# Kernel tuning notes

Measured on AMD Instinct MI355X. Metric: run time of the kernel, lower is better.

The kernel has to match this reference:

```python
import jax, jax.numpy as jnp
import numpy as np

B, T, V, E, Hd, NTAG = 16, 512, 32000, 100, 500, 32
PAD, SOS, EOS = 0, 1, 2
NEG = -10000.0


def _lstm_dir(xs, mask, Wih, Whh, b, h0, c0, reverse):
    # xs: [T,B,D]; mask: [T,B] bool. Packed-sequence semantics: at padded
    # steps the state is frozen and the output is zero (pad_packed fills 0).
    def step(carry, inp):
        h, c = carry
        x_t, m = inp
        g = x_t @ Wih.T + h @ Whh.T + b
        i, f, gg, o = jnp.split(g, 4, axis=-1)  # torch gate order i,f,g,o
        c_new = jax.nn.sigmoid(f) * c + jax.nn.sigmoid(i) * jnp.tanh(gg)
        h_new = jax.nn.sigmoid(o) * jnp.tanh(c_new)
        m_ = m[:, None]
        return (jnp.where(m_, h_new, h), jnp.where(m_, c_new, c)), jnp.where(m_, h_new, 0.0)
    _, ys = jax.lax.scan(step, (h0, c0), (xs, mask), reverse=reverse)
    return ys


def _forward(x, y0, embed_W, Wih0, Whh0, bih0, bhh0, Wih1, Whh1, bih1, bhh1, W_out, b_out, trans, h0, c0):
    maskb = x > 0                       # [B,T]
    maskf = maskb.astype(embed_W.dtype)
    mT = maskb.T                        # [T,B]
    xs = embed_W[x].transpose(1, 0, 2)  # [T,B,E]
    # layer 0 (bidirectional)
    f0 = _lstm_dir(xs, mT, Wih0[0], Whh0[0], bih0[0] + bhh0[0], h0[0], c0[0], False)
    b0 = _lstm_dir(xs, mT, Wih0[1], Whh0[1], bih0[1] + bhh0[1], h0[1], c0[1], True)
    l1 = jnp.concatenate([f0, b0], axis=-1)  # [T,B,1000]
    # layer 1 (dropout omitted: deterministic reference)
    f1 = _lstm_dir(l1, mT, Wih1[0], Whh1[0], bih1[0] + bhh1[0], h0[2], c0[2], False)
    b1 = _lstm_dir(l1, mT, Wih1[1], Whh1[1], bih1[1] + bhh1[1], h0[3], c0[3], True)
    hseq = jnp.concatenate([f1, b1], axis=-1).transpose(1, 0, 2)  # [B,T,1000]
    # emissions, masked exactly as in loss(): y = y * mask
    y = (hseq @ W_out.T + b_out) * maskf[:, :, None]  # [B,T,NTAG]
    # gold path score (crf_score_batch)
    y0e = jnp.concatenate([jnp.full((B, 1), SOS, y0.dtype), y0], axis=1)
    emit = jnp.take_along_axis(y, y0e[:, 1:, None], axis=2)[..., 0]
    tr = trans[y0e[:, 1:], y0e[:, :-1]] * maskf
    gold = jnp.sum(emit + tr, axis=1)  # [B]
    # log-partition (crf_forward_batch). Faithful to the original, including
    # the quirk that finished rows are overwritten with max_g score[b,g].
    init = jnp.full((B, NTAG), NEG, y.dtype).at[:, SOS].set(0.0)
    def step(score, inp):
        emit_t, m_t = inp  # [B,NTAG], [B]
        z = score[:, None, :] + trans[None, :, :] + emit_t[:, :, None]  # [B,F,G]
        new = jax.nn.logsumexp(z, axis=2)
        carry = jnp.broadcast_to(jnp.max(score, axis=1, keepdims=True), score.shape)
        return jnp.where(m_t[:, None], new, carry), None
    final, _ = jax.lax.scan(step, init, (y.transpose(1, 0, 2), mT))
    Z = jax.nn.logsumexp(final, axis=1)
    return jnp.mean(Z - gold)


def setup_inputs() -> dict:
    key = jax.random.key(0)
    ks = jax.random.split(key, 14)
    rng = np.random.default_rng(0)
    lengths = np.sort(rng.integers(T // 4, T + 1, size=B))[::-1]  # sorted desc (pack_padded)
    valid = np.arange(T)[None, :] < lengths[:, None]
    x = rng.integers(1, V, size=(B, T)) * valid
    y0 = rng.integers(3, NTAG, size=(B, T)) * valid
    rn = lambda k, s, sc=0.1: jax.random.normal(k, s, jnp.float32) * sc
    embed_W = rn(ks[0], (V, E)).at[0].set(0.0)  # padding_idx=0
    Wih0, Whh0 = rn(ks[1], (2, 4 * Hd, E)), rn(ks[2], (2, 4 * Hd, Hd))
    bih0, bhh0 = rn(ks[3], (2, 4 * Hd)), rn(ks[4], (2, 4 * Hd))
    Wih1, Whh1 = rn(ks[5], (2, 4 * Hd, 2 * Hd)), rn(ks[6], (2, 4 * Hd, Hd))
    bih1, bhh1 = rn(ks[7], (2, 4 * Hd)), rn(ks[8], (2, 4 * Hd))
    W_out, b_out = rn(ks[9], (NTAG, 2 * Hd)), rn(ks[10], (NTAG,))
    trans = jax.random.normal(ks[11], (NTAG, NTAG), jnp.float32)
    trans = trans.at[SOS, :].set(NEG).at[:, EOS].set(NEG).at[:, PAD].set(NEG).at[PAD, :].set(NEG)
    trans = trans.at[PAD, EOS].set(0.0).at[PAD, PAD].set(0.0)
    h0 = jax.random.normal(ks[12], (4, B, Hd), jnp.float32)
    c0 = jax.random.normal(ks[13], (4, B, Hd), jnp.float32)
    return dict(x=jnp.asarray(x, jnp.int32), y0=jnp.asarray(y0, jnp.int32), embed_W=embed_W,
                Wih0=Wih0, Whh0=Whh0, bih0=bih0, bhh0=bhh0, Wih1=Wih1, Whh1=Whh1,
                bih1=bih1, bhh1=bhh1, W_out=W_out, b_out=b_out, trans=trans, h0=h0, c0=c0)


def reference(x, y0, embed_W, Wih0, Whh0, bih0, bhh0, Wih1, Whh1, bih1, bhh1, W_out, b_out, trans, h0, c0):
    return _forward(x, y0, embed_W, Wih0, Whh0, bih0, bhh0, Wih1, Whh1, bih1, bhh1, W_out, b_out, trans, h0, c0)
```

## Files before the change

### kernel.cpp

```cpp
#include <hip/hip_runtime.h>
#include <hip/hip_fp16.h>
#include <math.h>

#define TT 512
#define BB 16
#define EE 100
#define HD 500
#define NEG (-10000.0f)
#define SENT64 0xFFFFFFFFFFFFFFFFull
#define SENT32 0xFFFFFFFFu

typedef __attribute__((ext_vector_type(8))) short short8;
typedef __attribute__((ext_vector_type(4))) float f32x4;
typedef __attribute__((ext_vector_type(4))) unsigned int u32x4;

__device__ inline short f2bf(float f) {
    unsigned u = __builtin_bit_cast(unsigned, f);
    unsigned r = (u + 0x7fffu + ((u >> 16) & 1u)) >> 16;
    return (short)r;
}
__device__ inline unsigned short f2h(float f) {
    __half h = __float2half(f);
    return __builtin_bit_cast(unsigned short, h);
}
__device__ inline float h2f(unsigned short u) {
    __half h = __builtin_bit_cast(__half, u);
    return __half2float(h);
}
__device__ inline float bf2f(unsigned short u) {
    return __builtin_bit_cast(float, ((unsigned)u) << 16);
}
__device__ inline float sigm_fast(float x) {
    return __builtin_amdgcn_rcpf(1.f + __expf(-x));
}
__device__ inline float tanh_fast(float x) {
    return 1.f - 2.f * __builtin_amdgcn_rcpf(__expf(2.f * x) + 1.f);
}
__device__ inline void store_u16_wt(unsigned short* p, unsigned short v) {
    asm volatile("global_store_short %0, %1, off sc0 sc1" :: "v"(p), "v"((unsigned)v) : "memory");
}

__global__ void maxlen_kernel(const int* __restrict__ x, int* __restrict__ out) {
    __shared__ int mx;
    int t = threadIdx.x;
    if (t == 0) mx = 1;
    __syncthreads();
    int any = 0;
    for (int b = 0; b < BB; ++b) any |= (x[b * TT + t] > 0);
    if (any) atomicMax(&mx, t + 1);
    __syncthreads();
    if (t == 0) out[0] = mx;
}

__global__ void sentfill_kernel(unsigned long long* __restrict__ p, int n,
                                int* __restrict__ cnt) {
    int i = blockIdx.x * 256 + threadIdx.x;
    if (i < n)
        __hip_atomic_store(p + i, SENT64, __ATOMIC_RELAXED, __HIP_MEMORY_SCOPE_AGENT);
    if (cnt && blockIdx.x == 0 && threadIdx.x < 128)
        __hip_atomic_store(cnt + threadIdx.x, 0, __ATOMIC_RELAXED, __HIP_MEMORY_SCOPE_AGENT);
}

__global__ void embed_kernel(const int* __restrict__ x, const float* __restrict__ EW,
                             unsigned short* __restrict__ XS) {
    int idx = blockIdx.x * 256 + threadIdx.x;
    int e = idx & 127;
    int r = idx >> 7;
    int t = r >> 4;
    int b = r & 15;
    unsigned short v = 0;
    if (e < EE) {
        int tok = x[b * TT + t];
        v = (unsigned short)f2bf(EW[(size_t)tok * EE + e]);
    }
    XS[idx] = v;
}

__global__ void wconv_kernel(const float* __restrict__ src, unsigned short* __restrict__ dst,
                             int Ksrc, int Kpad, int total) {
    int i = blockIdx.x * 256 + threadIdx.x;
    if (i >= total) return;
    int r = i / Kpad;
    int k = i - r * Kpad;
    dst[i] = (k < Ksrc) ? (unsigned short)f2bf(src[(size_t)r * Ksrc + k]) : 0;
}

__global__ void padzero_kernel(int* __restrict__ p) {
    int i = blockIdx.x * 256 + threadIdx.x;
    if (i >= 8192 * 12) return;
    int r = i / 12, c = i - r * 12;
    p[r * 512 + 500 + c] = 0;
}

__device__ __forceinline__ void gemm_body(
    const unsigned short* __restrict__ A, const unsigned short* __restrict__ W,
    const float* __restrict__ b1, const float* __restrict__ b2,
    unsigned short* __restrict__ C, int Kpad, int bx, int by, int z,
    int* gcnt) {
    __shared__ __align__(16) unsigned short AsS[128 * 40];
    __shared__ __align__(16) unsigned short WsS[64 * 40];
    const int tid = threadIdx.x;
    const int lane = tid & 63;
    const int w = tid >> 6;
    const int quad = lane >> 4;
    const int nl = lane & 15;
    const int bm0 = bx * 128;
    const int n0 = by * 64;

    const unsigned short* Wz = W + (size_t)z * 2000 * Kpad;
    unsigned short* Cz = C + (size_t)z * 8192 * 2000;
    const float* b1z = b1 + (size_t)z * 2000;
    const float* b2z = b2 + (size_t)z * 2000;

    f32x4 acc[2][4];
#pragma unroll
    for (int mt = 0; mt < 2; ++mt)
#pragma unroll
        for (int nt = 0; nt < 4; ++nt) acc[mt][nt] = (f32x4){0.f, 0.f, 0.f, 0.f};

    const int arow = tid >> 2;
    const int kc = tid & 3;
    const int wn = n0 + arow;
    const bool wok = (wn < 2000);

    const unsigned short* Ap0 = A + (size_t)(bm0 + arow) * Kpad + kc * 8;
    const unsigned short* Ap1 = A + (size_t)(bm0 + 64 + arow) * Kpad + kc * 8;
    const unsigned short* Wp  = Wz + (size_t)(wok ? wn : 0) * Kpad + kc * 8;

    short8 av0 = *(const short8*)(Ap0);
    short8 av1 = *(const short8*)(Ap1);
    short8 wv = {0, 0, 0, 0, 0, 0, 0, 0};
    if (wok) wv = *(const short8*)(Wp);

    for (int k0 = 0; k0 < Kpad; k0 += 32) {
        __syncthreads();
        *(short8*)&AsS[arow * 40 + kc * 8] = av0;
        *(short8*)&AsS[(64 + arow) * 40 + kc * 8] = av1;
        *(short8*)&WsS[arow * 40 + kc * 8] = wv;
        __syncthreads();

        if (k0 + 32 < Kpad) {
            av0 = *(const short8*)(Ap0 + k0 + 32);
            av1 = *(const short8*)(Ap1 + k0 + 32);
            if (wok) wv = *(const short8*)(Wp + k0 + 32);
        }

        short8 af[2], bfr[4];
#pragma unroll
        for (int mt = 0; mt < 2; ++mt)
            af[mt] = *(const short8*)&AsS[(w * 32 + mt * 16 + nl) * 40 + quad * 8];
#pragma unroll
        for (int nt = 0; nt < 4; ++nt)
            bfr[nt] = *(const short8*)&WsS[(nt * 16 + nl) * 40 + quad * 8];
#pragma unroll
        for (int mt = 0; mt < 2; ++mt)
#pragma unroll
            for (int nt = 0; nt < 4; ++nt)
                acc[mt][nt] = __builtin_amdgcn_mfma_f32_16x16x32_bf16(
                    af[mt], bfr[nt], acc[mt][nt], 0, 0, 0);
    }

    if (!gcnt) {
#pragma unroll
        for (int nt = 0; nt < 4; ++nt) {
            int n = n0 + nt * 16 + nl;
            if (n < 2000) {
                float bb = b1z[n] + b2z[n];
#pragma unroll
                for (int mt = 0; mt < 2; ++mt) {
                    int mbase = bm0 + w * 32 + mt * 16 + quad * 4;
#pragma unroll
                    for (int reg = 0; reg < 4; ++reg)
                        Cz[(size_t)(mbase + reg) * 2000 + n] = f2h(acc[mt][nt][reg] + bb);
                }
            }
        }
    } else {
#pragma unroll
        for (int nt = 0; nt < 4; ++nt) {
            int n = n0 + nt * 16 + nl;
            if (n < 2000) {
                float bb = b1z[n] + b2z[n];
#pragma unroll
                for (int mt = 0; mt < 2; ++mt) {
                    int mbase = bm0 + w * 32 + mt * 16 + quad * 4;
#pragma unroll
                    for (int reg = 0; reg < 4; ++reg)
                        store_u16_wt(&Cz[(size_t)(mbase + reg) * 2000 + n],
                                     f2h(acc[mt][nt][reg] + bb));
                }
            }
        }
        asm volatile("s_waitcnt vmcnt(0)" ::: "memory");
        __syncthreads();
        if (tid == 0)
            __hip_atomic_fetch_add(&gcnt[z * 64 + bx], 1,
                                   __ATOMIC_RELAXED, __HIP_MEMORY_SCOPE_AGENT);
    }
}

__global__ __launch_bounds__(256) void gemm_mfma(
    const unsigned short* __restrict__ A, const unsigned short* __restrict__ W,
    const float* __restrict__ b1, const float* __restrict__ b2,
    unsigned short* __restrict__ C, int Kpad) {
    gemm_body(A, W, b1, b2, C, Kpad, blockIdx.x, blockIdx.y, blockIdx.z, nullptr);
}

__device__ __forceinline__ void rec_body(
    const unsigned short* __restrict__ G, const float* __restrict__ Whh,
    const int* __restrict__ x, const float* __restrict__ h0,
    const float* __restrict__ c0, int layerbase,
    unsigned short* __restrict__ Hout, unsigned short* __restrict__ hseq,
    const int* __restrict__ mlen, int* gcnt, int blk)
{
    const int dir = blk >> 4;
    const int bsl = blk & 15;
    const int k0 = bsl * 32;
    const int tid = threadIdx.x;
    const int lane = tid & 63;
    const int w = tid >> 6;
    const int quad = lane >> 4;
    const int nl = lane & 15;
    const int L = mlen[0];

    const float* Wd = Whh + (size_t)dir * 2000 * HD;
    const unsigned short* Gd = G + (size_t)dir * TT * BB * 2000;
    unsigned short* hdir = hseq + (size_t)dir * (TT + 1) * 8192;

    __shared__ __align__(16) unsigned short hstage[8192];
    __shared__ float sg[4][32][17];

    short8 bf[2][16];
#pragma unroll
    for (int tl = 0; tl < 2; ++tl) {
        int tt = w * 2 + tl;
        int r = tt * 16 + nl;
        int g = r >> 5;
        int lkr = r & 31;
        int kk = k0 + lkr;
        const float* wrow = (kk < HD) ? (Wd + (size_t)(g * HD + kk) * HD) : (const float*)0;
#pragma unroll
        for (int ks = 0; ks < 16; ++ks) {
            int kg0 = ks * 32 + quad * 8;
            short8 v;
            if (wrow && kg0 + 8 <= HD) {
                float4 f0 = *(const float4*)(wrow + kg0);
                float4 f1 = *(const float4*)(wrow + kg0 + 4);
                v[0] = f2bf(f0.x); v[1] = f2bf(f0.y); v[2] = f2bf(f0.z); v[3] = f2bf(f0.w);
                v[4] = f2bf(f1.x); v[5] = f2bf(f1.y); v[6] = f2bf(f1.z); v[7] = f2bf(f1.w);
            } else {
#pragma unroll
                for (int j = 0; j < 8; ++j) {
                    int kg = kg0 + j;
                    float f = (wrow && kg < HD) ? wrow[kg] : 0.f;
                    v[j] = f2bf(f);
                }
            }
            bf[tl][ks] = v;
        }
    }

    const int lk = tid & 31;
    const int k  = k0 + lk;
    const bool kok = (k < HD);
    const int b0v = tid >> 5;
    const int b1v = 8 + (tid >> 5);
    float h_st[2] = {0.f, 0.f}, c_st[2] = {0.f, 0.f};
    if (kok) {
        size_t base0 = (size_t)(layerbase + dir) * BB * HD + (size_t)b0v * HD + k;
        size_t base1 = (size_t)(layerbase + dir) * BB * HD + (size_t)b1v * HD + k;
        h_st[0] = h0[base0]; c_st[0] = c0[base0];
        h_st[1] = h0[base1]; c_st[1] = c0[base1];
    }

    {
        int i0 = (int)(unsigned short)f2bf(kok ? h_st[0] : 0.f);
        int i1 = (int)(unsigned short)f2bf(kok ? h_st[1] : 0.f);
        int a0 = __shfl_down(i0, 1), c0s = __shfl_down(i0, 2), d0 = __shfl_down(i0, 3);
        int a1 = __shfl_down(i1, 1), c1s = __shfl_down(i1, 2), d1 = __shfl_down(i1, 3);
        if ((lk & 3) == 0) {
            unsigned long long p0 = (unsigned long long)(unsigned)(i0 | (a0 << 16))
                                  | ((unsigned long long)(unsigned)(c0s | (d0 << 16)) << 32);
            unsigned long long p1 = (unsigned long long)(unsigned)(i1 | (a1 << 16))
                                  | ((unsigned long long)(unsigned)(c1s | (d1 << 16)) << 32);
            int idx0 = bsl * 512 + (b0v + 16 * (lk >> 3)) * 8 + (lk & 7);
            int idx1 = bsl * 512 + (b1v + 16 * (lk >> 3)) * 8 + (lk & 7);
            __hip_atomic_store((unsigned long long*)(hdir + idx0), p0,
                               __ATOMIC_RELAXED, __HIP_MEMORY_SCOPE_AGENT);
            __hip_atomic_store((unsigned long long*)(hdir + idx1), p1,
                               __ATOMIC_RELAXED, __HIP_MEMORY_SCOPE_AGENT);
        }
    }

    unsigned g00 = 0, g01 = 0, g02 = 0, g03 = 0, g10 = 0, g11 = 0, g12 = 0, g13 = 0;
    int m[2]; m[0] = m[1] = 0;
    int lastTile = -1;

    {
        int t = dir ? (L - 1) : 0;
        if (gcnt) {
            int tile = dir * 64 + (t >> 3);
            while (__hip_atomic_load(&gcnt[tile], __ATOMIC_RELAXED,
                                     __HIP_MEMORY_SCOPE_AGENT) < 32) {}
            lastTile = tile;
        }
        if (kok) {
            const unsigned short* gr0 = Gd + ((size_t)t * BB + b0v) * 2000 + k;
            const unsigned short* gr1 = Gd + ((size_t)t * BB + b1v) * 2000 + k;
            asm volatile(
                "global_load_ushort %0, %8, off sc0 sc1\n\t"
                "global_load_ushort %1, %8, off offset:1000 sc0 sc1\n\t"
                "global_load_ushort %2, %8, off offset:2000 sc0 sc1\n\t"
                "global_load_ushort %3, %8, off offset:3000 sc0 sc1\n\t"
                "global_load_ushort %4, %9, off sc0 sc1\n\t"
                "global_load_ushort %5, %9, off offset:1000 sc0 sc1\n\t"
                "global_load_ushort %6, %9, off offset:2000 sc0 sc1\n\t"
                "global_load_ushort %7, %9, off offset:3000 sc0 sc1"
                : "=&v"(g00), "=&v"(g01), "=&v"(g02), "=&v"(g03),
                  "=&v"(g10), "=&v"(g11), "=&v"(g12), "=&v"(g13)
                : "v"(gr0), "v"(gr1) : "memory");
            m[0] = x[b0v * TT + t] > 0;
            m[1] = x[b1v * TT + t] > 0;
        }
    }

    for (int s = 0; s < L; ++s) {
        const int t = dir ? (L - 1 - s) : s;
        const unsigned short* bufr = hdir + (size_t)s * 8192;
        unsigned short* bufw = hdir + (size_t)(s + 1) * 8192;

        {
            const unsigned short* p0 = bufr + (tid +   0) * 8;
            const unsigned short* p1 = bufr + (tid + 256) * 8;
            const unsigned short* p2 = bufr + (tid + 512) * 8;
            const unsigned short* p3 = bufr + (tid + 768) * 8;
            u32x4 c0v, c1v, c2v, c3v;
            for (;;) {
                asm volatile(
                    "global_load_dwordx4 %0, %12, off sc0 sc1\n\t"
                    "global_load_dwordx4 %1, %13, off sc0 sc1\n\t"
                    "global_load_dwordx4 %2, %14, off sc0 sc1\n\t"
                    "global_load_dwordx4 %3, %15, off sc0 sc1\n\t"
                    "s_waitcnt vmcnt(0)"
                    : "=&v"(c0v), "=&v"(c1v), "=&v"(c2v), "=&v"(c3v),
                      "+v"(g00), "+v"(g01), "+v"(g02), "+v"(g03),
                      "+v"(g10), "+v"(g11), "+v"(g12), "+v"(g13)
                    : "v"(p0), "v"(p1), "v"(p2), "v"(p3)
                    : "memory");
                unsigned bad = 0;
#pragma unroll
                for (int q = 0; q < 4; ++q)
                    bad |= (c0v[q] == SENT32) | (c1v[q] == SENT32)
                         | (c2v[q] == SENT32) | (c3v[q] == SENT32);
                if (!bad) break;
            }
            *(u32x4*)&hstage[(tid +   0) * 8] = c0v;
            *(u32x4*)&hstage[(tid + 256) * 8] = c1v;
            *(u32x4*)&hstage[(tid + 512) * 8] = c2v;
            *(u32x4*)&hstage[(tid + 768) * 8] = c3v;
        }
        __syncthreads();

        f32x4 acc0 = {0.f, 0.f, 0.f, 0.f};
        f32x4 acc1 = {0.f, 0.f, 0.f, 0.f};
#pragma unroll
        for (int ks = 0; ks < 16; ++ks) {
            short8 a = *(const short8*)&hstage[ks * 512 + lane * 8];
            acc0 = __builtin_amdgcn_mfma_f32_16x16x32_bf16(a, bf[0][ks], acc0, 0, 0, 0);
            acc1 = __builtin_amdgcn_mfma_f32_16x16x32_bf16(a, bf[1][ks], acc1, 0, 0, 0);
        }

        {
            int r0 = (w * 2 + 0) * 16 + nl;
            int r1 = (w * 2 + 1) * 16 + nl;
            int g0r = r0 >> 5, lk0 = r0 & 31;
            int g1r = r1 >> 5, lk1 = r1 & 31;
#pragma unroll
            for (int reg = 0; reg < 4; ++reg) {
                int b = quad * 4 + reg;
                sg[g0r][lk0][b] = acc0[reg];
                sg[g1r][lk1][b] = acc1[reg];
            }
        }
        __syncthreads();

        int i0 = 0, i1 = 0;
        if (kok) {
            {
                float si  = sg[0][lk][b0v] + h2f((unsigned short)g00);
                float sf  = sg[1][lk][b0v] + h2f((unsigned short)g01);
                float sgg = sg[2][lk][b0v] + h2f((unsigned short)g02);
                float so  = sg[3][lk][b0v] + h2f((unsigned short)g03);
                float c_new = sigm_fast(sf) * c_st[0] + sigm_fast(si) * tanh_fast(sgg);
                float h_new = sigm_fast(so) * tanh_fast(c_new);
                if (m[0]) { h_st[0] = h_new; c_st[0] = c_new; }
            }
            {
                float si  = sg[0][lk][b1v] + h2f((unsigned short)g10);
                float sf  = sg[1][lk][b1v] + h2f((unsigned short)g11);
                float sgg = sg[2][lk][b1v] + h2f((unsigned short)g12);
                float so  = sg[3][lk][b1v] + h2f((unsigned short)g13);
                float c_new = sigm_fast(sf) * c_st[1] + sigm_fast(si) * tanh_fast(sgg);
                float h_new = sigm_fast(so) * tanh_fast(c_new);
                if (m[1]) { h_st[1] = h_new; c_st[1] = c_new; }
            }
            i0 = (int)(unsigned short)f2bf(h_st[0]);
            i1 = (int)(unsigned short)f2bf(h_st[1]);
        }

        {
            int a0 = __shfl_down(i0, 1), c0s = __shfl_down(i0, 2), d0 = __shfl_down(i0, 3);
            int a1 = __shfl_down(i1, 1), c1s = __shfl_down(i1, 2), d1 = __shfl_down(i1, 3);
            if ((lk & 3) == 0) {
                unsigned long long p0 = (unsigned long long)(unsigned)(i0 | (a0 << 16))
                                      | ((unsigned long long)(unsigned)(c0s | (d0 << 16)) << 32);
                unsigned long long p1 = (unsigned long long)(unsigned)(i1 | (a1 << 16))
                                      | ((unsigned long long)(unsigned)(c1s | (d1 << 16)) << 32);
                int idx0 = bsl * 512 + (b0v + 16 * (lk >> 3)) * 8 + (lk & 7);
                int idx1 = bsl * 512 + (b1v + 16 * (lk >> 3)) * 8 + (lk & 7);
                __hip_atomic_store((unsigned long long*)(bufw + idx0), p0,
                                   __ATOMIC_RELAXED, __HIP_MEMORY_SCOPE_AGENT);
                __hip_atomic_store((unsigned long long*)(bufw + idx1), p1,
                                   __ATOMIC_RELAXED, __HIP_MEMORY_SCOPE_AGENT);
            }
        }

        if (kok) {
            Hout[((size_t)t * BB + b0v) * 1024 + dir * HD + k] =
                (unsigned short)(m[0] ? i0 : 0);
            Hout[((size_t)t * BB + b1v) * 1024 + dir * HD + k] =
                (unsigned short)(m[1] ? i1 : 0);
        }

        if (s + 1 < L) {
            int tn = dir ? (L - 2 - s) : (s + 1);
            if (gcnt) {
                int tile = dir * 64 + (tn >> 3);
                if (tile != lastTile) {
                    while (__hip_atomic_load(&gcnt[tile], __ATOMIC_RELAXED,
                                             __HIP_MEMORY_SCOPE_AGENT) < 32) {}
                    lastTile = tile;
                }
            }
            if (kok) {
                const unsigned short* gr0 = Gd + ((size_t)tn * BB + b0v) * 2000 + k;
                const unsigned short* gr1 = Gd + ((size_t)tn * BB + b1v) * 2000 + k;
                asm volatile(
                    "global_load_ushort %0, %8, off sc0 sc1\n\t"
                    "global_load_ushort %1, %8, off offset:1000 sc0 sc1\n\t"
                    "global_load_ushort %2, %8, off offset:2000 sc0 sc1\n\t"
                    "global_load_ushort %3, %8, off offset:3000 sc0 sc1\n\t"
                    "global_load_ushort %4, %9, off sc0 sc1\n\t"
                    "global_load_ushort %5, %9, off offset:1000 sc0 sc1\n\t"
                    "global_load_ushort %6, %9, off offset:2000 sc0 sc1\n\t"
                    "global_load_ushort %7, %9, off offset:3000 sc0 sc1"
                    : "=&v"(g00), "=&v"(g01), "=&v"(g02), "=&v"(g03),
                      "=&v"(g10), "=&v"(g11), "=&v"(g12), "=&v"(g13)
                    : "v"(gr0), "v"(gr1) : "memory");
                m[0] = x[b0v * TT + tn] > 0;
                m[1] = x[b1v * TT + tn] > 0;
            }
        }
    }
}

__global__ __launch_bounds__(256, 1) void rec10_kernel(
    const unsigned short* __restrict__ G, const float* __restrict__ Whh,
    const int* __restrict__ x, const float* __restrict__ h0,
    const float* __restrict__ c0, int layerbase,
    unsigned short* __restrict__ Hout, unsigned short* __restrict__ hseq,
    const int* __restrict__ mlen) {
    rec_body(G, Whh, x, h0, c0, layerbase, Hout, hseq, mlen, nullptr, blockIdx.x);
}

__global__ __launch_bounds__(256, 1) void fused1_kernel(
    unsigned short* __restrict__ Gh, const float* __restrict__ Whh1,
    const int* __restrict__ x, const float* __restrict__ h0,
    const float* __restrict__ c0, unsigned short* __restrict__ HSb,
    unsigned short* __restrict__ hseq, const int* __restrict__ mlen,
    const unsigned short* __restrict__ H0b, const unsigned short* __restrict__ Wb1,
    const float* __restrict__ bih1, const float* __restrict__ bhh1,
    int* gcnt) {
    int bid = blockIdx.x;
    if (bid < 32) {
        rec_body(Gh, Whh1, x, h0, c0, 2, HSb, hseq, mlen, gcnt, bid);
    } else {
        int gx = bid - 32;
        int z = gx & 1;
        int rem = gx >> 1;
        int bx = rem >> 5;
        int by = rem & 31;
        if (z) bx = 63 - bx;
        gemm_body(H0b, Wb1, bih1, bhh1, Gh, 1024, bx, by, z, gcnt);
    }
}

__global__ __launch_bounds__(256) void outproj_kernel(
    const unsigned short* __restrict__ HS, const float* __restrict__ Wo,
    const float* __restrict__ bo, const int* __restrict__ x,
    float* __restrict__ Y) {
    __shared__ float wlds[8 * 1000];
    const int bid = blockIdx.x;
    const int tid = threadIdx.x;
    const int rblk = bid >> 2;
    const int n0 = (bid & 3) * 8;
    for (int i = tid; i < 8000; i += 256) {
        int nn = i / 1000;
        int q = i - nn * 1000;
        wlds[i] = Wo[(size_t)(n0 + nn) * 1000 + q];
    }
    __syncthreads();
    const int r = rblk * 32 + (tid >> 3);
    const int n = n0 + (tid & 7);
    const int t = r >> 4;
    const int b = r & 15;
    float out = 0.f;
    if (x[b * TT + t] > 0) {
        const unsigned short* h = HS + (size_t)r * 1024;
        const float* wrow = &wlds[(tid & 7) * 1000];
        float s = 0.f;
#pragma unroll 4
        for (int q = 0; q < 1000; q += 8) {
            short8 hv = *(const short8*)(h + q);
            float4 w0 = *(const float4*)(wrow + q);
            float4 w1 = *(const float4*)(wrow + q + 4);
            s += bf2f((unsigned short)hv[0]) * w0.x + bf2f((unsigned short)hv[1]) * w0.y
               + bf2f((unsigned short)hv[2]) * w0.z + bf2f((unsigned short)hv[3]) * w0.w
               + bf2f((unsigned short)hv[4]) * w1.x + bf2f((unsigned short)hv[5]) * w1.y
               + bf2f((unsigned short)hv[6]) * w1.z + bf2f((unsigned short)hv[7]) * w1.w;
        }
        out = s + bo[n];
    }
    Y[(size_t)r * 32 + n] = out;
}

__global__ __launch_bounds__(1024) void crf_kernel(
    const float* __restrict__ Y, const int* __restrict__ x, const int* __restrict__ y0,
    const float* __restrict__ trans, float* __restrict__ out_pb) {
    int b = blockIdx.x;
    int tid = threadIdx.x;
    int i = tid >> 5;
    int j = tid & 31;
    float tr_ij = trans[i * 32 + j];

    __shared__ float scb[2][32];
    __shared__ float wred[16];
    __shared__ float goldS;

    float gp = 0.f;
    if (tid < TT) {
        int t = tid;
        int xm = x[b * TT + t];
        float mf = (xm > 0) ? 1.f : 0.f;
        int ynext = y0[b * TT + t];
        int yprev = (t == 0) ? 1 : y0[b * TT + t - 1];
        gp = Y[((size_t)t * BB + b) * 32 + ynext] + trans[ynext * 32 + yprev] * mf;
    }
#pragma unroll
    for (int d = 32; d >= 1; d >>= 1) gp += __shfl_down(gp, d);
    if ((tid & 63) == 0) wred[tid >> 6] = gp;
    __syncthreads();
    if (tid == 0) {
        float s = 0.f;
        for (int ww = 0; ww < 16; ++ww) s += wred[ww];
        goldS = s;
    }
    if (tid < 32) scb[0][tid] = (tid == 1) ? 0.f : NEG;
    __syncthreads();

    int cur = 0;
    float emit_c = Y[((size_t)0 * BB + b) * 32 + i];
    int mm_c = x[b * TT + 0] > 0;
    for (int t = 0; t < TT; ++t) {
        float emit_n = 0.f;
        int mm_n = 0;
        if (t + 1 < TT) {
            emit_n = Y[((size_t)(t + 1) * BB + b) * 32 + i];
            mm_n = x[b * TT + t + 1] > 0;
        }
        float sj = scb[cur][j];
        float z = sj + tr_ij;
        float mx = z;
#pragma unroll
        for (int d = 16; d >= 1; d >>= 1) mx = fmaxf(mx, __shfl_xor(mx, d));
        float e = __expf(z - mx);
#pragma unroll
        for (int d = 16; d >= 1; d >>= 1) e += __shfl_xor(e, d);
        float cm = sj;
#pragma unroll
        for (int d = 16; d >= 1; d >>= 1) cm = fmaxf(cm, __shfl_xor(cm, d));
        float newv = emit_c + mx + __logf(e);
        if (j == 0) scb[cur ^ 1][i] = mm_c ? newv : cm;
        __syncthreads();
        cur ^= 1;
        emit_c = emit_n;
        mm_c = mm_n;
    }

    if (tid < 32) {
        float v = scb[cur][tid];
        float mx = v;
#pragma unroll
        for (int d = 16; d >= 1; d >>= 1) mx = fmaxf(mx, __shfl_xor(mx, d));
        float e = __expf(v - mx);
#pragma unroll
        for (int d = 16; d >= 1; d >>= 1) e += __shfl_xor(e, d);
        if (tid == 0) out_pb[b] = (mx + __logf(e)) - goldS;
    }
}

__global__ void final_kernel(const float* __restrict__ out_pb, float* __restrict__ out) {
    if (threadIdx.x == 0 && blockIdx.x == 0) {
        float s = 0.f;
        for (int b = 0; b < BB; ++b) s += out_pb[b];
        out[0] = s / (float)BB;
    }
}

extern "C" void kernel_launch(void* const* d_in, const int* in_sizes, int n_in,
                              void* d_out, int out_size, void* d_ws, size_t ws_size,
                              hipStream_t stream) {
    const int*   x     = (const int*)d_in[0];
    const int*   y0    = (const int*)d_in[1];
    const float* EW    = (const float*)d_in[2];
    const float* Wih0  = (const float*)d_in[3];
    const float* Whh0  = (const float*)d_in[4];
    const float* bih0  = (const float*)d_in[5];
    const float* bhh0  = (const float*)d_in[6];
    const float* Wih1  = (const float*)d_in[7];
    const float* Whh1  = (const float*)d_in[8];
    const float* bih1  = (const float*)d_in[9];
    const float* bhh1  = (const float*)d_in[10];
    const float* Wo    = (const float*)d_in[11];
    const float* bo    = (const float*)d_in[12];
    const float* trans = (const float*)d_in[13];
    const float* h0    = (const float*)d_in[14];
    const float* c0    = (const float*)d_in[15];

    float* ws = (float*)d_ws;
    unsigned short* XS = (unsigned short*)ws;
    float* Y      = ws;
    float* crfbuf = ws + 262144;
    unsigned short* Gh   = (unsigned short*)(ws + 524288);
    unsigned short* H0b  = (unsigned short*)(ws + 16908288);
    unsigned short* HSb  = (unsigned short*)(ws + 21102592);
    unsigned short* Wb0  = (unsigned short*)(ws + 25296896);
    unsigned short* Wb1  = (unsigned short*)(ws + 25552896);
    unsigned short* hseq = (unsigned short*)(ws + 27600896);
    int* mlen     = (int*)(ws + 31803392);
    int* gcnt     = (int*)(ws + 31803393);
    const int nsent64 = 2 * (TT + 1) * 8192 / 4;

    maxlen_kernel<<<1, 512, 0, stream>>>(x, mlen);
    sentfill_kernel<<<(nsent64 + 255) / 256, 256, 0, stream>>>((unsigned long long*)hseq, nsent64, gcnt);

    embed_kernel<<<4096, 256, 0, stream>>>(x, EW, XS);
    wconv_kernel<<<(512000 + 255) / 256, 256, 0, stream>>>(Wih0, Wb0, 100, 128, 512000);
    wconv_kernel<<<(4096000 + 255) / 256, 256, 0, stream>>>(Wih1, Wb1, 1000, 1024, 4096000);

    gemm_mfma<<<dim3(64, 32, 2), 256, 0, stream>>>(XS, Wb0, bih0, bhh0, Gh, 128);
    padzero_kernel<<<(98304 + 255) / 256, 256, 0, stream>>>((int*)H0b);

    rec10_kernel<<<32, 256, 0, stream>>>(Gh, Whh0, x, h0, c0, 0, H0b, hseq, mlen);

    sentfill_kernel<<<(nsent64 + 255) / 256, 256, 0, stream>>>((unsigned long long*)hseq, nsent64, gcnt);

    fused1_kernel<<<32 + 4096, 256, 0, stream>>>(Gh, Whh1, x, h0, c0, HSb, hseq, mlen,
                                                 H0b, Wb1, bih1, bhh1, gcnt);

    outproj_kernel<<<1024, 256, 0, stream>>>(HSb, Wo, bo, x, Y);

    crf_kernel<<<BB, 1024, 0, stream>>>(Y, x, y0, trans, crfbuf);

    final_kernel<<<1, 64, 0, stream>>>(crfbuf, (float*)d_out);
}
```

Baseline: 2.616 ms.

## Merge prep kernels, overlap layer-0 GEMM with recurrence, interleave gate columns

Combines maxlen, sentinel fill, embedding, weight conversion and pad zeroing into one prep launch. Layer 0 now uses the same fused GEMM-plus-recurrence kernel as layer 1, with counter-based handoff, so the input projection overlaps the recurrence. The GEMM output is stored with the four gates interleaved per hidden unit, so the recurrence fetches them with one 8-byte load instead of four 2-byte loads. The cost is scattered 2-byte write-through stores in the GEMM epilogue and a dependency on the gcnt counters being reset correctly between layers.

```diff
diff --git a/kernel.cpp b/kernel.cpp
--- a/kernel.cpp
+++ b/kernel.cpp
@@ -13,6 +13,7 @@
 typedef __attribute__((ext_vector_type(8))) short short8;
 typedef __attribute__((ext_vector_type(4))) float f32x4;
 typedef __attribute__((ext_vector_type(4))) unsigned int u32x4;
+typedef __attribute__((ext_vector_type(2))) unsigned int u32x2;
 
 __device__ inline short f2bf(float f) {
     unsigned u = __builtin_bit_cast(unsigned, f);
@@ -40,16 +41,83 @@
     asm volatile("global_store_short %0, %1, off sc0 sc1" :: "v"(p), "v"((unsigned)v) : "memory");
 }
 
-__global__ void maxlen_kernel(const int* __restrict__ x, int* __restrict__ out) {
-    __shared__ int mx;
-    int t = threadIdx.x;
-    if (t == 0) mx = 1;
-    __syncthreads();
-    int any = 0;
-    for (int b = 0; b < BB; ++b) any |= (x[b * TT + t] > 0);
-    if (any) atomicMax(&mx, t + 1);
-    __syncthreads();
-    if (t == 0) out[0] = mx;
+#define NSENT64B 8208
+#define NEMB     4096
+#define NWC0     2000
+#define NWC1     16000
+#define NPAD     384
+__global__ __launch_bounds__(256) void prep_kernel(
+    const int* __restrict__ x, int* __restrict__ mlen,
+    unsigned long long* __restrict__ sentp, int* __restrict__ gcnt,
+    const float* __restrict__ EW, unsigned short* __restrict__ XS,
+    const float* __restrict__ Wih0, unsigned short* __restrict__ Wb0,
+    const float* __restrict__ Wih1, unsigned short* __restrict__ Wb1,
+    int* __restrict__ H0pad) {
+    int bid = blockIdx.x;
+    int tid = threadIdx.x;
+    if (bid == 0) {
+        __shared__ int mx;
+        if (tid == 0) mx = 1;
+        if (tid < 128)
+            __hip_atomic_store(gcnt + tid, 0, __ATOMIC_RELAXED, __HIP_MEMORY_SCOPE_AGENT);
+        __syncthreads();
+        int any0 = 0, any1 = 0;
+        for (int b = 0; b < BB; ++b) {
+            any0 |= (x[b * TT + tid] > 0);
+            any1 |= (x[b * TT + tid + 256] > 0);
+        }
+        if (any0) atomicMax(&mx, tid + 1);
+        if (any1) atomicMax(&mx, tid + 257);
+        __syncthreads();
+        if (tid == 0) mlen[0] = mx;
+        return;
+    }
+    bid -= 1;
+    if (bid < NSENT64B) {
+        int i = bid * 256 + tid;
+        if (i < 2101248)
+            __hip_atomic_store(sentp + i, SENT64, __ATOMIC_RELAXED, __HIP_MEMORY_SCOPE_AGENT);
+        return;
+    }
+    bid -= NSENT64B;
+    if (bid < NEMB) {
+        int idx = bid * 256 + tid;
+        int e = idx & 127;
+        int r = idx >> 7;
+        int t = r >> 4;
+        int b = r & 15;
+        unsigned short v = 0;
+        if (e < EE) {
+            int tok = x[b * TT + t];
+            v = (unsigned short)f2bf(EW[(size_t)tok * EE + e]);
+        }
+        XS[idx] = v;
+        return;
+    }
+    bid -= NEMB;
+    if (bid < NWC0) {
+        int i = bid * 256 + tid;
+        int r = i >> 7;
+        int k = i & 127;
+        Wb0[i] = (k < 100) ? (unsigned short)f2bf(Wih0[(size_t)r * 100 + k]) : 0;
+        return;
+    }
+    bid -= NWC0;
+    if (bid < NWC1) {
+        int i = bid * 256 + tid;
+        int r = i >> 10;
+        int k = i & 1023;
+        Wb1[i] = (k < 1000) ? (unsigned short)f2bf(Wih1[(size_t)r * 1000 + k]) : 0;
+        return;
+    }
+    bid -= NWC1;
+    {
+        int i = bid * 256 + tid;
+        if (i < 8192 * 12) {
+            int r = i / 12, c = i - r * 12;
+            H0pad[r * 512 + 500 + c] = 0;
+        }
+    }
 }
 
 __global__ void sentfill_kernel(unsigned long long* __restrict__ p, int n,
@@ -59,37 +127,6 @@
         __hip_atomic_store(p + i, SENT64, __ATOMIC_RELAXED, __HIP_MEMORY_SCOPE_AGENT);
     if (cnt && blockIdx.x == 0 && threadIdx.x < 128)
         __hip_atomic_store(cnt + threadIdx.x, 0, __ATOMIC_RELAXED, __HIP_MEMORY_SCOPE_AGENT);
-}
-
-__global__ void embed_kernel(const int* __restrict__ x, const float* __restrict__ EW,
-                             unsigned short* __restrict__ XS) {
-    int idx = blockIdx.x * 256 + threadIdx.x;
-    int e = idx & 127;
-    int r = idx >> 7;
-    int t = r >> 4;
-    int b = r & 15;
-    unsigned short v = 0;
-    if (e < EE) {
-        int tok = x[b * TT + t];
-        v = (unsigned short)f2bf(EW[(size_t)tok * EE + e]);
-    }
-    XS[idx] = v;
-}
-
-__global__ void wconv_kernel(const float* __restrict__ src, unsigned short* __restrict__ dst,
-                             int Ksrc, int Kpad, int total) {
-    int i = blockIdx.x * 256 + threadIdx.x;
-    if (i >= total) return;
-    int r = i / Kpad;
-    int k = i - r * Kpad;
-    dst[i] = (k < Ksrc) ? (unsigned short)f2bf(src[(size_t)r * Ksrc + k]) : 0;
-}
-
-__global__ void padzero_kernel(int* __restrict__ p) {
-    int i = blockIdx.x * 256 + threadIdx.x;
-    if (i >= 8192 * 12) return;
-    int r = i / 12, c = i - r * 12;
-    p[r * 512 + 500 + c] = 0;
 }
 
 __device__ __forceinline__ void gemm_body(
@@ -160,50 +197,28 @@
                     af[mt], bfr[nt], acc[mt][nt], 0, 0, 0);
     }
 
-    if (!gcnt) {
-#pragma unroll
-        for (int nt = 0; nt < 4; ++nt) {
-            int n = n0 + nt * 16 + nl;
-            if (n < 2000) {
-                float bb = b1z[n] + b2z[n];
-#pragma unroll
-                for (int mt = 0; mt < 2; ++mt) {
-                    int mbase = bm0 + w * 32 + mt * 16 + quad * 4;
-#pragma unroll
-                    for (int reg = 0; reg < 4; ++reg)
-                        Cz[(size_t)(mbase + reg) * 2000 + n] = f2h(acc[mt][nt][reg] + bb);
-                }
-            }
-        }
-    } else {
-#pragma unroll
-        for (int nt = 0; nt < 4; ++nt) {
-            int n = n0 + nt * 16 + nl;
-            if (n < 2000) {
-                float bb = b1z[n] + b2z[n];
-#pragma unroll
-                for (int mt = 0; mt < 2; ++mt) {
-                    int mbase = bm0 + w * 32 + mt * 16 + quad * 4;
-#pragma unroll
-                    for (int reg = 0; reg < 4; ++reg)
-                        store_u16_wt(&Cz[(size_t)(mbase + reg) * 2000 + n],
-                                     f2h(acc[mt][nt][reg] + bb));
-                }
-            }
-        }
-        asm volatile("s_waitcnt vmcnt(0)" ::: "memory");
-        __syncthreads();
-        if (tid == 0)
-            __hip_atomic_fetch_add(&gcnt[z * 64 + bx], 1,
-                                   __ATOMIC_RELAXED, __HIP_MEMORY_SCOPE_AGENT);
-    }
-}
-
-__global__ __launch_bounds__(256) void gemm_mfma(
-    const unsigned short* __restrict__ A, const unsigned short* __restrict__ W,
-    const float* __restrict__ b1, const float* __restrict__ b2,
-    unsigned short* __restrict__ C, int Kpad) {
-    gemm_body(A, W, b1, b2, C, Kpad, blockIdx.x, blockIdx.y, blockIdx.z, nullptr);
+#pragma unroll
+    for (int nt = 0; nt < 4; ++nt) {
+        int n = n0 + nt * 16 + nl;
+        if (n < 2000) {
+            float bb = b1z[n] + b2z[n];
+            int g = (n >= 1000) ? ((n >= 1500) ? 3 : 2) : ((n >= 500) ? 1 : 0);
+            int col = (n - g * 500) * 4 + g;
+#pragma unroll
+            for (int mt = 0; mt < 2; ++mt) {
+                int mbase = bm0 + w * 32 + mt * 16 + quad * 4;
+#pragma unroll
+                for (int reg = 0; reg < 4; ++reg)
+                    store_u16_wt(&Cz[(size_t)(mbase + reg) * 2000 + col],
+                                 f2h(acc[mt][nt][reg] + bb));
+            }
+        }
+    }
+    asm volatile("s_waitcnt vmcnt(0)" ::: "memory");
+    __syncthreads();
+    if (tid == 0)
+        __hip_atomic_fetch_add(&gcnt[z * 64 + bx], 1,
+                               __ATOMIC_RELAXED, __HIP_MEMORY_SCOPE_AGENT);
 }
 
 __device__ __forceinline__ void rec_body(
@@ -292,7 +307,7 @@
         }
     }
 
-    unsigned g00 = 0, g01 = 0, g02 = 0, g03 = 0, g10 = 0, g11 = 0, g12 = 0, g13 = 0;
+    u32x2 ga = {0, 0}, gb = {0, 0};
     int m[2]; m[0] = m[1] = 0;
     int lastTile = -1;
 
@@ -305,20 +320,12 @@
             lastTile = tile;
         }
         if (kok) {
-            const unsigned short* gr0 = Gd + ((size_t)t * BB + b0v) * 2000 + k;
-            const unsigned short* gr1 = Gd + ((size_t)t * BB + b1v) * 2000 + k;
+            const unsigned short* gr0 = Gd + ((size_t)t * BB + b0v) * 2000 + (size_t)k * 4;
+            const unsigned short* gr1 = Gd + ((size_t)t * BB + b1v) * 2000 + (size_t)k * 4;
             asm volatile(
-                "global_load_ushort %0, %8, off sc0 sc1\n\t"
-                "global_load_ushort %1, %8, off offset:1000 sc0 sc1\n\t"
-                "global_load_ushort %2, %8, off offset:2000 sc0 sc1\n\t"
-                "global_load_ushort %3, %8, off offset:3000 sc0 sc1\n\t"
-                "global_load_ushort %4, %9, off sc0 sc1\n\t"
-                "global_load_ushort %5, %9, off offset:1000 sc0 sc1\n\t"
-                "global_load_ushort %6, %9, off offset:2000 sc0 sc1\n\t"
-                "global_load_ushort %7, %9, off offset:3000 sc0 sc1"
-                : "=&v"(g00), "=&v"(g01), "=&v"(g02), "=&v"(g03),
-                  "=&v"(g10), "=&v"(g11), "=&v"(g12), "=&v"(g13)
-                : "v"(gr0), "v"(gr1) : "memory");
+                "global_load_dwordx2 %0, %2, off sc0 sc1\n\t"
+                "global_load_dwordx2 %1, %3, off sc0 sc1"
+                : "=&v"(ga), "=&v"(gb) : "v"(gr0), "v"(gr1) : "memory");
             m[0] = x[b0v * TT + t] > 0;
             m[1] = x[b1v * TT + t] > 0;
         }
@@ -337,14 +344,13 @@
             u32x4 c0v, c1v, c2v, c3v;
             for (;;) {
                 asm volatile(
-                    "global_load_dwordx4 %0, %12, off sc0 sc1\n\t"
-                    "global_load_dwordx4 %1, %13, off sc0 sc1\n\t"
-                    "global_load_dwordx4 %2, %14, off sc0 sc1\n\t"
-                    "global_load_dwordx4 %3, %15, off sc0 sc1\n\t"
+                    "global_load_dwordx4 %0, %6, off sc0 sc1\n\t"
+                    "global_load_dwordx4 %1, %7, off sc0 sc1\n\t"
+                    "global_load_dwordx4 %2, %8, off sc0 sc1\n\t"
+                    "global_load_dwordx4 %3, %9, off sc0 sc1\n\t"
                     "s_waitcnt vmcnt(0)"
                     : "=&v"(c0v), "=&v"(c1v), "=&v"(c2v), "=&v"(c3v),
-                      "+v"(g00), "+v"(g01), "+v"(g02), "+v"(g03),
-                      "+v"(g10), "+v"(g11), "+v"(g12), "+v"(g13)
+                      "+v"(ga), "+v"(gb)
                     : "v"(p0), "v"(p1), "v"(p2), "v"(p3)
                     : "memory");
                 unsigned bad = 0;
@@ -387,19 +393,21 @@
         int i0 = 0, i1 = 0;
         if (kok) {
             {
-                float si  = sg[0][lk][b0v] + h2f((unsigned short)g00);
-                float sf  = sg[1][lk][b0v] + h2f((unsigned short)g01);
-                float sgg = sg[2][lk][b0v] + h2f((unsigned short)g02);
-                float so  = sg[3][lk][b0v] + h2f((unsigned short)g03);
+                unsigned w0 = ga[0], w1 = ga[1];
+                float si  = sg[0][lk][b0v] + h2f((unsigned short)(w0 & 0xffffu));
+                float sf  = sg[1][lk][b0v] + h2f((unsigned short)(w0 >> 16));
+                float sgg = sg[2][lk][b0v] + h2f((unsigned short)(w1 & 0xffffu));
+                float so  = sg[3][lk][b0v] + h2f((unsigned short)(w1 >> 16));
                 float c_new = sigm_fast(sf) * c_st[0] + sigm_fast(si) * tanh_fast(sgg);
                 float h_new = sigm_fast(so) * tanh_fast(c_new);
                 if (m[0]) { h_st[0] = h_new; c_st[0] = c_new; }
             }
             {
-                float si  = sg[0][lk][b1v] + h2f((unsigned short)g10);
-                float sf  = sg[1][lk][b1v] + h2f((unsigned short)g11);
-                float sgg = sg[2][lk][b1v] + h2f((unsigned short)g12);
-                float so  = sg[3][lk][b1v] + h2f((unsigned short)g13);
+                unsigned w0 = gb[0], w1 = gb[1];
+                float si  = sg[0][lk][b1v] + h2f((unsigned short)(w0 & 0xffffu));
+                float sf  = sg[1][lk][b1v] + h2f((unsigned short)(w0 >> 16));
+                float sgg = sg[2][lk][b1v] + h2f((unsigned short)(w1 & 0xffffu));
+                float so  = sg[3][lk][b1v] + h2f((unsigned short)(w1 >> 16));
                 float c_new = sigm_fast(sf) * c_st[1] + sigm_fast(si) * tanh_fast(sgg);
                 float h_new = sigm_fast(so) * tanh_fast(c_new);
                 if (m[1]) { h_st[1] = h_new; c_st[1] = c_new; }
@@ -443,20 +451,12 @@
                 }
             }
             if (kok) {
-                const unsigned short* gr0 = Gd + ((size_t)tn * BB + b0v) * 2000 + k;
-                const unsigned short* gr1 = Gd + ((size_t)tn * BB + b1v) * 2000 + k;
+                const unsigned short* gr0 = Gd + ((size_t)tn * BB + b0v) * 2000 + (size_t)k * 4;
+                const unsigned short* gr1 = Gd + ((size_t)tn * BB + b1v) * 2000 + (size_t)k * 4;
                 asm volatile(
-                    "global_load_ushort %0, %8, off sc0 sc1\n\t"
-                    "global_load_ushort %1, %8, off offset:1000 sc0 sc1\n\t"
-                    "global_load_ushort %2, %8, off offset:2000 sc0 sc1\n\t"
-                    "global_load_ushort %3, %8, off offset:3000 sc0 sc1\n\t"
-                    "global_load_ushort %4, %9, off sc0 sc1\n\t"
-                    "global_load_ushort %5, %9, off offset:1000 sc0 sc1\n\t"
-                    "global_load_ushort %6, %9, off offset:2000 sc0 sc1\n\t"
-                    "global_load_ushort %7, %9, off offset:3000 sc0 sc1"
-                    : "=&v"(g00), "=&v"(g01), "=&v"(g02), "=&v"(g03),
-                      "=&v"(g10), "=&v"(g11), "=&v"(g12), "=&v"(g13)
-                    : "v"(gr0), "v"(gr1) : "memory");
+                    "global_load_dwordx2 %0, %2, off sc0 sc1\n\t"
+                    "global_load_dwordx2 %1, %3, off sc0 sc1"
+                    : "=&v"(ga), "=&v"(gb) : "v"(gr0), "v"(gr1) : "memory");
                 m[0] = x[b0v * TT + tn] > 0;
                 m[1] = x[b1v * TT + tn] > 0;
             }
@@ -464,26 +464,17 @@
     }
 }
 
-__global__ __launch_bounds__(256, 1) void rec10_kernel(
-    const unsigned short* __restrict__ G, const float* __restrict__ Whh,
-    const int* __restrict__ x, const float* __restrict__ h0,
-    const float* __restrict__ c0, int layerbase,
+__global__ __launch_bounds__(256, 1) void fused_kernel(
+    const unsigned short* __restrict__ A, const unsigned short* __restrict__ Wb,
+    const float* __restrict__ b1, const float* __restrict__ b2,
+    unsigned short* __restrict__ Gh, int Kpad,
+    const float* __restrict__ Whh, const int* __restrict__ x,
+    const float* __restrict__ h0, const float* __restrict__ c0, int layerbase,
     unsigned short* __restrict__ Hout, unsigned short* __restrict__ hseq,
-    const int* __restrict__ mlen) {
-    rec_body(G, Whh, x, h0, c0, layerbase, Hout, hseq, mlen, nullptr, blockIdx.x);
-}
-
-__global__ __launch_bounds__(256, 1) void fused1_kernel(
-    unsigned short* __restrict__ Gh, const float* __restrict__ Whh1,
-    const int* __restrict__ x, const float* __restrict__ h0,
-    const float* __restrict__ c0, unsigned short* __restrict__ HSb,
-    unsigned short* __restrict__ hseq, const int* __restrict__ mlen,
-    const unsigned short* __restrict__ H0b, const unsigned short* __restrict__ Wb1,
-    const float* __restrict__ bih1, const float* __restrict__ bhh1,
-    int* gcnt) {
+    const int* __restrict__ mlen, int* gcnt) {
     int bid = blockIdx.x;
     if (bid < 32) {
-        rec_body(Gh, Whh1, x, h0, c0, 2, HSb, hseq, mlen, gcnt, bid);
+        rec_body(Gh, Whh, x, h0, c0, layerbase, Hout, hseq, mlen, gcnt, bid);
     } else {
         int gx = bid - 32;
         int z = gx & 1;
@@ -491,7 +482,7 @@
         int bx = rem >> 5;
         int by = rem & 31;
         if (z) bx = 63 - bx;
-        gemm_body(H0b, Wb1, bih1, bhh1, Gh, 1024, bx, by, z, gcnt);
+        gemm_body(A, Wb, b1, b2, Gh, Kpad, bx, by, z, gcnt);
     }
 }
 
@@ -651,22 +642,17 @@
     int* gcnt     = (int*)(ws + 31803393);
     const int nsent64 = 2 * (TT + 1) * 8192 / 4;
 
-    maxlen_kernel<<<1, 512, 0, stream>>>(x, mlen);
+    const int nprep = 1 + NSENT64B + NEMB + NWC0 + NWC1 + NPAD;
+    prep_kernel<<<nprep, 256, 0, stream>>>(x, mlen, (unsigned long long*)hseq, gcnt,
+                                           EW, XS, Wih0, Wb0, Wih1, Wb1, (int*)H0b);
+
+    fused_kernel<<<32 + 4096, 256, 0, stream>>>(XS, Wb0, bih0, bhh0, Gh, 128,
+                                                Whh0, x, h0, c0, 0, H0b, hseq, mlen, gcnt);
+
     sentfill_kernel<<<(nsent64 + 255) / 256, 256, 0, stream>>>((unsigned long long*)hseq, nsent64, gcnt);
 
-    embed_kernel<<<4096, 256, 0, stream>>>(x, EW, XS);
-    wconv_kernel<<<(512000 + 255) / 256, 256, 0, stream>>>(Wih0, Wb0, 100, 128, 512000);
-    wconv_kernel<<<(4096000 + 255) / 256, 256, 0, stream>>>(Wih1, Wb1, 1000, 1024, 4096000);
-
-    gemm_mfma<<<dim3(64, 32, 2), 256, 0, stream>>>(XS, Wb0, bih0, bhh0, Gh, 128);
-    padzero_kernel<<<(98304 + 255) / 256, 256, 0, stream>>>((int*)H0b);
-
-    rec10_kernel<<<32, 256, 0, stream>>>(Gh, Whh0, x, h0, c0, 0, H0b, hseq, mlen);
-
-    sentfill_kernel<<<(nsent64 + 255) / 256, 256, 0, stream>>>((unsigned long long*)hseq, nsent64, gcnt);
-
-    fused1_kernel<<<32 + 4096, 256, 0, stream>>>(Gh, Whh1, x, h0, c0, HSb, hseq, mlen,
-                                                 H0b, Wb1, bih1, bhh1, gcnt);
+    fused_kernel<<<32 + 4096, 256, 0, stream>>>(H0b, Wb1, bih1, bhh1, Gh, 1024,
+                                                Whh1, x, h0, c0, 2, HSb, hseq, mlen, gcnt);
 
     outproj_kernel<<<1024, 256, 0, stream>>>(HSb, Wo, bo, x, Y);
 
```

After: 2.679 ms. +2.4%, slower.
